# Kernel optimization log

Measured on AMD Instinct MI355X. Metric: run time of the kernel, lower is better.

## Reference

```python
import jax, jax.numpy as jnp
import numpy as np

B, H, L = 8, 256, 16384

def setup_inputs() -> dict:
    key = jax.random.key(0)
    k1, k2, k3 = jax.random.split(key, 3)
    u = jax.random.normal(k1, (B, H, L), dtype=jnp.float32)
    # SSM convolution kernel (H, L); small scale to keep tanh unsaturated
    k = jax.random.normal(k2, (H, L), dtype=jnp.float32) * 0.02
    # D feedthrough parameter (H, H); forward only uses its diagonal via einsum 'hh,bhl->bhl'
    D = jax.random.normal(k3, (H, H), dtype=jnp.float32)
    return {"u": u, "k": k, "D": D}

def reference(u, k, D):
    # circular FFT convolution: y = ifft(fft(u) * fft(k)).real
    u_s = jnp.fft.fft(u, axis=-1)          # (B,H,L) complex64
    k_s = jnp.fft.fft(k, axis=-1)          # (H,L)   complex64
    y = jnp.fft.ifft(u_s * k_s[None], axis=-1).real
    # D feedthrough: einsum 'hh,bhl->bhl' uses only diag(D)
    y = y + jnp.einsum('hh,bhl->bhl', D, u)
    return jnp.tanh(y)
```

## Files before the change

### kernel.cpp

```cpp
#include <hip/hip_runtime.h>
#include <math.h>

#define FFT_N 16384
#define NT 512
#define B_DIM 8
#define H_DIM 256

#define REGION 2048
#define RW (REGION + (REGION >> 5))
#define PAD(x) ((x) + ((x) >> 5))

#define WAVE_LDS_FENCE() do {                                   \
    __builtin_amdgcn_sched_barrier(0);                          \
    asm volatile("s_waitcnt lgkmcnt(0)" ::: "memory");          \
    __builtin_amdgcn_sched_barrier(0);                          \
} while (0)

__device__ __forceinline__ float2 cmul(float2 a, float2 b) {
    return make_float2(a.x * b.x - a.y * b.y, a.x * b.y + a.y * b.x);
}
__device__ __forceinline__ float2 cadd(float2 a, float2 b) { return make_float2(a.x + b.x, a.y + b.y); }
__device__ __forceinline__ float2 csub(float2 a, float2 b) { return make_float2(a.x - b.x, a.y - b.y); }
__device__ __forceinline__ float2 mulnegi(float2 z) { return make_float2(z.y, -z.x); }
__device__ __forceinline__ float2 mulposi(float2 z) { return make_float2(-z.y, z.x); }

__device__ __forceinline__ void bfly4(float2& a, float2& b, float2& c, float2& d,
                                      float2 w1, float2 w2, float2 w3) {
    float2 apc = cadd(a, c), amc = csub(a, c);
    float2 bpd = cadd(b, d), bmd = csub(b, d);
    float2 nib = mulnegi(bmd);
    a = cadd(apc, bpd);
    b = cmul(csub(apc, bpd), w2);
    c = cmul(cadd(amc, nib), w1);
    d = cmul(csub(amc, nib), w3);
}
__device__ __forceinline__ void bfly4_nw(float2& a, float2& b, float2& c, float2& d) {
    float2 apc = cadd(a, c), amc = csub(a, c);
    float2 bpd = cadd(b, d), bmd = csub(b, d);
    float2 nib = mulnegi(bmd);
    a = cadd(apc, bpd);
    b = csub(apc, bpd);
    c = cadd(amc, nib);
    d = csub(amc, nib);
}
__device__ __forceinline__ void ibfly4(float2& a, float2& b, float2& c, float2& d,
                                       float2 w1t, float2 w2t) {
    float2 w1 = make_float2(w1t.x, -w1t.y);
    float2 w2 = make_float2(w2t.x, -w2t.y);
    float2 bt = cmul(b, w2), dt = cmul(d, w2);
    float2 A = cadd(a, bt), Bb = csub(a, bt);
    float2 C = cadd(c, dt), Dd = csub(c, dt);
    float2 Cw = cmul(C, w1);
    float2 Dw = mulposi(cmul(Dd, w1));
    a = cadd(A, Cw);  c = csub(A, Cw);
    b = cadd(Bb, Dw); d = csub(Bb, Dw);
}
__device__ __forceinline__ void ibfly4_nw(float2& a, float2& b, float2& c, float2& d) {
    float2 A = cadd(a, b), Bb = csub(a, b);
    float2 C = cadd(c, d), Dd = csub(c, d);
    float2 Dw = mulposi(Dd);
    a = cadd(A, C);  c = csub(A, C);
    b = cadd(Bb, Dw); d = csub(Bb, Dw);
}

__device__ __forceinline__ void fwd_g01_half(float2 rh[16], const int t, const int par,
                                             const float2* __restrict__ tw) {
#pragma unroll
    for (int m0 = 0; m0 < 4; ++m0) {
        const int i = t + 512 * par + 1024 * m0;
        bfly4(rh[m0], rh[m0 + 4], rh[m0 + 8], rh[m0 + 12], tw[i], tw[2 * i], tw[3 * i]);
    }
    {
        const int ig = (t + 512 * par) * 4;
        const float2 w1 = tw[ig], w2 = tw[2 * ig], w3 = tw[3 * ig];
#pragma unroll
        for (int a = 0; a < 4; ++a)
            bfly4(rh[4 * a], rh[4 * a + 1], rh[4 * a + 2], rh[4 * a + 3], w1, w2, w3);
    }
}
__device__ __forceinline__ void inv_g01_half(float2 rh[16], const int t, const int par,
                                             const float2* __restrict__ tw) {
    {
        const int ig = (t + 512 * par) * 4;
        const float2 w1 = tw[ig], w2 = tw[2 * ig];
#pragma unroll
        for (int a = 0; a < 4; ++a)
            ibfly4(rh[4 * a], rh[4 * a + 1], rh[4 * a + 2], rh[4 * a + 3], w1, w2);
    }
#pragma unroll
    for (int m0 = 0; m0 < 4; ++m0) {
        const int i = t + 512 * par + 1024 * m0;
        ibfly4(rh[m0], rh[m0 + 4], rh[m0 + 8], rh[m0 + 12], tw[i], tw[2 * i]);
    }
}

__device__ __forceinline__ void fwd_mid_half(float2 rh[16], float* ldsx, float* ldsy,
                                             const int w, const int l, const int s,
                                             const float2* __restrict__ tw) {
#pragma unroll
    for (int jj = 0; jj < 16; ++jj) {
        const int a = w * RW + PAD(1024 * s + 64 * jj + l);
        rh[jj].x = ldsx[a]; rh[jj].y = ldsy[a];
    }
#pragma unroll
    for (int j0 = 0; j0 < 4; ++j0) {
        const int i1 = 1024 * j0 + 16 * l;
        bfly4(rh[j0], rh[j0 + 4], rh[j0 + 8], rh[j0 + 12], tw[i1], tw[2 * i1], tw[3 * i1]);
    }
    {
        const int i2 = 64 * l;
        const float2 w1 = tw[i2], w2 = tw[2 * i2], w3 = tw[3 * i2];
#pragma unroll
        for (int g = 0; g < 4; ++g)
            bfly4(rh[4 * g], rh[4 * g + 1], rh[4 * g + 2], rh[4 * g + 3], w1, w2, w3);
    }
#pragma unroll
    for (int jj = 0; jj < 16; ++jj) {
        const int a = w * RW + PAD(1024 * s + 64 * jj + l);
        ldsx[a] = rh[jj].x; ldsy[a] = rh[jj].y;
    }
    WAVE_LDS_FENCE();
    {
        const int lo = 64 * (l >> 2) + (l & 3);
#pragma unroll
        for (int jj = 0; jj < 16; ++jj) {
            const int a = w * RW + PAD(1024 * s + lo + 4 * jj);
            rh[jj].x = ldsx[a]; rh[jj].y = ldsy[a];
        }
    }
#pragma unroll
    for (int j0 = 0; j0 < 4; ++j0) {
        const int i3 = 1024 * j0 + 256 * (l & 3);
        bfly4(rh[j0], rh[j0 + 4], rh[j0 + 8], rh[j0 + 12], tw[i3], tw[2 * i3], tw[3 * i3]);
    }
    {
        const int i4 = 1024 * (l & 3);
        const float2 w1 = tw[i4], w2 = tw[2 * i4], w3 = tw[3 * i4];
#pragma unroll
        for (int g = 0; g < 4; ++g)
            bfly4(rh[4 * g], rh[4 * g + 1], rh[4 * g + 2], rh[4 * g + 3], w1, w2, w3);
    }
    {
        const int lo = 64 * (l >> 2) + (l & 3);
#pragma unroll
        for (int jj = 0; jj < 16; ++jj) {
            const int a = w * RW + PAD(1024 * s + lo + 4 * jj);
            ldsx[a] = rh[jj].x; ldsy[a] = rh[jj].y;
        }
    }
    WAVE_LDS_FENCE();
#pragma unroll
    for (int jj = 0; jj < 16; ++jj) {
        const int a = w * RW + PAD(1024 * s + 16 * l + jj);
        rh[jj].x = ldsx[a]; rh[jj].y = ldsy[a];
    }
#pragma unroll
    for (int g = 0; g < 4; ++g)
        bfly4_nw(rh[4 * g], rh[4 * g + 1], rh[4 * g + 2], rh[4 * g + 3]);
}

__device__ __forceinline__ void conv_mid_fused(float* ldsx, float* ldsy,
                                               const int t, const int w, const int l,
                                               const float4* __restrict__ kf4,
                                               const float invN,
                                               const float2* __restrict__ tw) {
    float2 r0[16], r1[16];
#pragma unroll
    for (int jj = 0; jj < 16; ++jj) {
        const int a0 = w * RW + PAD(64 * jj + l);
        const int a1 = w * RW + PAD(1024 + 64 * jj + l);
        r0[jj].x = ldsx[a0]; r0[jj].y = ldsy[a0];
        r1[jj].x = ldsx[a1]; r1[jj].y = ldsy[a1];
    }
#pragma unroll
    for (int j0 = 0; j0 < 4; ++j0) {
        const int i1 = 1024 * j0 + 16 * l;
        const float2 w1 = tw[i1], w2 = tw[2 * i1], w3 = tw[3 * i1];
        bfly4(r0[j0], r0[j0 + 4], r0[j0 + 8], r0[j0 + 12], w1, w2, w3);
        bfly4(r1[j0], r1[j0 + 4], r1[j0 + 8], r1[j0 + 12], w1, w2, w3);
    }
    {
        const int i2 = 64 * l;
        const float2 w1 = tw[i2], w2 = tw[2 * i2], w3 = tw[3 * i2];
#pragma unroll
        for (int g = 0; g < 4; ++g) {
            bfly4(r0[4 * g], r0[4 * g + 1], r0[4 * g + 2], r0[4 * g + 3], w1, w2, w3);
            bfly4(r1[4 * g], r1[4 * g + 1], r1[4 * g + 2], r1[4 * g + 3], w1, w2, w3);
        }
    }
#pragma unroll
    for (int jj = 0; jj < 16; ++jj) {
        const int a0 = w * RW + PAD(64 * jj + l);
        const int a1 = w * RW + PAD(1024 + 64 * jj + l);
        ldsx[a0] = r0[jj].x; ldsy[a0] = r0[jj].y;
        ldsx[a1] = r1[jj].x; ldsy[a1] = r1[jj].y;
    }
    WAVE_LDS_FENCE();
    {
        const int lo = 64 * (l >> 2) + (l & 3);
#pragma unroll
        for (int jj = 0; jj < 16; ++jj) {
            const int a0 = w * RW + PAD(lo + 4 * jj);
            const int a1 = w * RW + PAD(1024 + lo + 4 * jj);
            r0[jj].x = ldsx[a0]; r0[jj].y = ldsy[a0];
            r1[jj].x = ldsx[a1]; r1[jj].y = ldsy[a1];
        }
    }
#pragma unroll
    for (int j0 = 0; j0 < 4; ++j0) {
        const int i3 = 1024 * j0 + 256 * (l & 3);
        const float2 w1 = tw[i3], w2 = tw[2 * i3], w3 = tw[3 * i3];
        bfly4(r0[j0], r0[j0 + 4], r0[j0 + 8], r0[j0 + 12], w1, w2, w3);
        bfly4(r1[j0], r1[j0 + 4], r1[j0 + 8], r1[j0 + 12], w1, w2, w3);
    }
    {
        const int i4 = 1024 * (l & 3);
        const float2 w1 = tw[i4], w2 = tw[2 * i4], w3 = tw[3 * i4];
#pragma unroll
        for (int g = 0; g < 4; ++g) {
            bfly4(r0[4 * g], r0[4 * g + 1], r0[4 * g + 2], r0[4 * g + 3], w1, w2, w3);
            bfly4(r1[4 * g], r1[4 * g + 1], r1[4 * g + 2], r1[4 * g + 3], w1, w2, w3);
        }
    }
    {
        const int lo = 64 * (l >> 2) + (l & 3);
#pragma unroll
        for (int jj = 0; jj < 16; ++jj) {
            const int a0 = w * RW + PAD(lo + 4 * jj);
            const int a1 = w * RW + PAD(1024 + lo + 4 * jj);
            ldsx[a0] = r0[jj].x; ldsy[a0] = r0[jj].y;
            ldsx[a1] = r1[jj].x; ldsy[a1] = r1[jj].y;
        }
    }
    WAVE_LDS_FENCE();
#pragma unroll
    for (int jj = 0; jj < 16; ++jj) {
        const int a0 = w * RW + PAD(16 * l + jj);
        const int a1 = w * RW + PAD(1024 + 16 * l + jj);
        r0[jj].x = ldsx[a0]; r0[jj].y = ldsy[a0];
        r1[jj].x = ldsx[a1]; r1[jj].y = ldsy[a1];
    }
#pragma unroll
    for (int g = 0; g < 4; ++g) {
        bfly4_nw(r0[4 * g], r0[4 * g + 1], r0[4 * g + 2], r0[4 * g + 3]);
        bfly4_nw(r1[4 * g], r1[4 * g + 1], r1[4 * g + 2], r1[4 * g + 3]);
    }
#pragma unroll
    for (int q = 0; q < 8; ++q) {
        const float4 k0 = kf4[16 * t + q];
        const float4 k1 = kf4[16 * t + 8 + q];
        float2 z;
        z = r0[2 * q];
        r0[2 * q]     = make_float2((z.x * k0.x - z.y * k0.y) * invN, (z.x * k0.y + z.y * k0.x) * invN);
        z = r0[2 * q + 1];
        r0[2 * q + 1] = make_float2((z.x * k0.z - z.y * k0.w) * invN, (z.x * k0.w + z.y * k0.z) * invN);
        z = r1[2 * q];
        r1[2 * q]     = make_float2((z.x * k1.x - z.y * k1.y) * invN, (z.x * k1.y + z.y * k1.x) * invN);
        z = r1[2 * q + 1];
        r1[2 * q + 1] = make_float2((z.x * k1.z - z.y * k1.w) * invN, (z.x * k1.w + z.y * k1.z) * invN);
    }
#pragma unroll
    for (int g = 0; g < 4; ++g) {
        ibfly4_nw(r0[4 * g], r0[4 * g + 1], r0[4 * g + 2], r0[4 * g + 3]);
        ibfly4_nw(r1[4 * g], r1[4 * g + 1], r1[4 * g + 2], r1[4 * g + 3]);
    }
#pragma unroll
    for (int jj = 0; jj < 16; ++jj) {
        const int a0 = w * RW + PAD(16 * l + jj);
        const int a1 = w * RW + PAD(1024 + 16 * l + jj);
        ldsx[a0] = r0[jj].x; ldsy[a0] = r0[jj].y;
        ldsx[a1] = r1[jj].x; ldsy[a1] = r1[jj].y;
    }
    WAVE_LDS_FENCE();
    {
        const int lo = 64 * (l >> 2) + (l & 3);
#pragma unroll
        for (int jj = 0; jj < 16; ++jj) {
            const int a0 = w * RW + PAD(lo + 4 * jj);
            const int a1 = w * RW + PAD(1024 + lo + 4 * jj);
            r0[jj].x = ldsx[a0]; r0[jj].y = ldsy[a0];
            r1[jj].x = ldsx[a1]; r1[jj].y = ldsy[a1];
        }
    }
    {
        const int i4 = 1024 * (l & 3);
        const float2 w1 = tw[i4], w2 = tw[2 * i4];
#pragma unroll
        for (int g = 0; g < 4; ++g) {
            ibfly4(r0[4 * g], r0[4 * g + 1], r0[4 * g + 2], r0[4 * g + 3], w1, w2);
            ibfly4(r1[4 * g], r1[4 * g + 1], r1[4 * g + 2], r1[4 * g + 3], w1, w2);
        }
    }
#pragma unroll
    for (int j0 = 0; j0 < 4; ++j0) {
        const int i3 = 1024 * j0 + 256 * (l & 3);
        const float2 w1 = tw[i3], w2 = tw[2 * i3];
        ibfly4(r0[j0], r0[j0 + 4], r0[j0 + 8], r0[j0 + 12], w1, w2);
        ibfly4(r1[j0], r1[j0 + 4], r1[j0 + 8], r1[j0 + 12], w1, w2);
    }
    {
        const int lo = 64 * (l >> 2) + (l & 3);
#pragma unroll
        for (int jj = 0; jj < 16; ++jj) {
            const int a0 = w * RW + PAD(lo + 4 * jj);
            const int a1 = w * RW + PAD(1024 + lo + 4 * jj);
            ldsx[a0] = r0[jj].x; ldsy[a0] = r0[jj].y;
            ldsx[a1] = r1[jj].x; ldsy[a1] = r1[jj].y;
        }
    }
    WAVE_LDS_FENCE();
#pragma unroll
    for (int jj = 0; jj < 16; ++jj) {
        const int a0 = w * RW + PAD(64 * jj + l);
        const int a1 = w * RW + PAD(1024 + 64 * jj + l);
        r0[jj].x = ldsx[a0]; r0[jj].y = ldsy[a0];
        r1[jj].x = ldsx[a1]; r1[jj].y = ldsy[a1];
    }
    {
        const int i2 = 64 * l;
        const float2 w1 = tw[i2], w2 = tw[2 * i2];
#pragma unroll
        for (int g = 0; g < 4; ++g) {
            ibfly4(r0[4 * g], r0[4 * g + 1], r0[4 * g + 2], r0[4 * g + 3], w1, w2);
            ibfly4(r1[4 * g], r1[4 * g + 1], r1[4 * g + 2], r1[4 * g + 3], w1, w2);
        }
    }
#pragma unroll
    for (int j0 = 0; j0 < 4; ++j0) {
        const int i1 = 1024 * j0 + 16 * l;
        const float2 w1 = tw[i1], w2 = tw[2 * i1];
        ibfly4(r0[j0], r0[j0 + 4], r0[j0 + 8], r0[j0 + 12], w1, w2);
        ibfly4(r1[j0], r1[j0 + 4], r1[j0 + 8], r1[j0 + 12], w1, w2);
    }
#pragma unroll
    for (int jj = 0; jj < 16; ++jj) {
        const int a0 = w * RW + PAD(64 * jj + l);
        const int a1 = w * RW + PAD(1024 + 64 * jj + l);
        ldsx[a0] = r0[jj].x; ldsy[a0] = r0[jj].y;
        ldsx[a1] = r1[jj].x; ldsy[a1] = r1[jj].y;
    }
}

__device__ __forceinline__ float ftanh(float x) {
    float e = __expf(2.0f * x);
    return 1.0f - 2.0f * __builtin_amdgcn_rcpf(e + 1.0f);
}

__global__ void twiddle_init(float2* __restrict__ tw) {
    int t = blockIdx.x * blockDim.x + threadIdx.x;
    if (t < FFT_N) {
        float ang = -2.0f * 3.14159265358979323846f * (float)t / (float)FFT_N;
        float sv, cv;
        sincosf(ang, &sv, &cv);
        tw[t] = make_float2(cv, sv);
    }
}

__global__ __launch_bounds__(NT) void kfft_kernel(const float* __restrict__ k,
                                                  const float* __restrict__ D,
                                                  const float2* __restrict__ tw,
                                                  float2* __restrict__ Kf) {
    __shared__ float ldsx[8 * RW];
    __shared__ float ldsy[8 * RW];
    const int h = blockIdx.x;
    const int t = threadIdx.x;
    const int w = t >> 6, l = t & 63;
    const float* krow = k + (size_t)h * FFT_N;
    const float dh = D[h * (H_DIM + 1)];
#pragma unroll
    for (int par = 0; par < 2; ++par) {
        float2 rh[16];
#pragma unroll
        for (int m = 0; m < 16; ++m)
            rh[m] = make_float2(krow[t + 512 * par + 1024 * m], 0.f);
        if (par == 0 && t == 0) rh[0].x += dh;
        fwd_g01_half(rh, t, par, tw);
#pragma unroll
        for (int m = 0; m < 16; ++m) {
            const int e = t + 512 * par + 1024 * m;
            const int a = (e >> 11) * RW + PAD(e & 2047);
            ldsx[a] = rh[m].x; ldsy[a] = rh[m].y;
        }
    }
    __syncthreads();
    float4* out4 = (float4*)(Kf + (size_t)h * FFT_N);
#pragma unroll
    for (int s = 0; s < 2; ++s) {
        float2 rh[16];
        fwd_mid_half(rh, ldsx, ldsy, w, l, s, tw);
#pragma unroll
        for (int q = 0; q < 8; ++q)
            out4[16 * t + 8 * s + q] =
                make_float4(rh[2 * q].x, rh[2 * q].y, rh[2 * q + 1].x, rh[2 * q + 1].y);
    }
}

__global__ __launch_bounds__(NT) void conv_kernel(const float* __restrict__ u,
                                                  const float2* __restrict__ tw,
                                                  const float2* __restrict__ Kf,
                                                  float* __restrict__ out) {
    __shared__ float ldsx[8 * RW];
    __shared__ float ldsy[8 * RW];
    const int raw = blockIdx.x;
    const int vb = ((raw & 7) << 7) + (raw >> 3);
    const int h = vb >> 2;
    const int p = vb & 3;
    const int t = threadIdx.x;
    const int w = t >> 6, l = t & 63;
    const size_t row0 = ((size_t)(2 * p) * H_DIM + h) * FFT_N;
    const size_t row1 = row0 + (size_t)H_DIM * FFT_N;
    const float* u0 = u + row0;
    const float* u1 = u + row1;

#pragma unroll
    for (int par = 0; par < 2; ++par) {
        float2 rh[16];
#pragma unroll
        for (int m = 0; m < 16; ++m) {
            const int n = t + 512 * par + 1024 * m;
            rh[m] = make_float2(u0[n], u1[n]);
        }
        fwd_g01_half(rh, t, par, tw);
#pragma unroll
        for (int m = 0; m < 16; ++m) {
            const int e = t + 512 * par + 1024 * m;
            const int a = (e >> 11) * RW + PAD(e & 2047);
            ldsx[a] = rh[m].x; ldsy[a] = rh[m].y;
        }
    }
    __syncthreads();

    conv_mid_fused(ldsx, ldsy, t, w, l,
                   (const float4*)(Kf + (size_t)h * FFT_N), 1.0f / (float)FFT_N, tw);
    __syncthreads();

    float* o0 = out + row0;
    float* o1 = out + row1;
#pragma unroll
    for (int par = 0; par < 2; ++par) {
        float2 rh[16];
#pragma unroll
        for (int m = 0; m < 16; ++m) {
            const int e = t + 512 * par + 1024 * m;
            const int a = (e >> 11) * RW + PAD(e & 2047);
            rh[m].x = ldsx[a]; rh[m].y = ldsy[a];
        }
        inv_g01_half(rh, t, par, tw);
#pragma unroll
        for (int m = 0; m < 16; ++m) {
            const int n = t + 512 * par + 1024 * m;
            o0[n] = ftanh(rh[m].x);
            o1[n] = ftanh(rh[m].y);
        }
    }
}

extern "C" void kernel_launch(void* const* d_in, const int* in_sizes, int n_in,
                              void* d_out, int out_size, void* d_ws, size_t ws_size,
                              hipStream_t stream) {
    const float* u = (const float*)d_in[0];
    const float* k = (const float*)d_in[1];
    const float* D = (const float*)d_in[2];
    float* out = (float*)d_out;

    float2* tw = (float2*)d_ws;
    float2* Kf = tw + FFT_N;

    twiddle_init<<<FFT_N / 256, 256, 0, stream>>>(tw);
    kfft_kernel<<<H_DIM, NT, 0, stream>>>(k, D, tw, Kf);
    conv_kernel<<<(B_DIM / 2) * H_DIM, NT, 0, stream>>>(u, tw, Kf, out);
}
```

Baseline: 200.4 us.

## Drop wave LDS fences, fold 1/N into kernel spectrum, prefetch Kf early

Removes the explicit per-wave s_waitcnt/sched_barrier fences between LDS write and read phases and leaves ordering to the compiler's own waitcnt insertion. Moves the 1/N scaling into the precomputed kernel spectrum so the pointwise multiply in the conv kernel does fewer multiplies. Issues early touch loads of the Kf row at kernel start, kept alive with an empty asm, so the spectrum is pulled into cache while the forward FFT runs. Removing the fences relies on the compiler to keep correct LDS ordering within a wave, and the prefetch adds a few registers.

After: 209.8 us. +4.7%, slower.

```diff
diff --git a/kernel.cpp b/kernel.cpp
--- a/kernel.cpp
+++ b/kernel.cpp
@@ -10,11 +10,6 @@
 #define RW (REGION + (REGION >> 5))
 #define PAD(x) ((x) + ((x) >> 5))
 
-#define WAVE_LDS_FENCE() do {                                   \
-    __builtin_amdgcn_sched_barrier(0);                          \
-    asm volatile("s_waitcnt lgkmcnt(0)" ::: "memory");          \
-    __builtin_amdgcn_sched_barrier(0);                          \
-} while (0)
 
 __device__ __forceinline__ float2 cmul(float2 a, float2 b) {
     return make_float2(a.x * b.x - a.y * b.y, a.x * b.y + a.y * b.x);
@@ -119,7 +114,6 @@
         const int a = w * RW + PAD(1024 * s + 64 * jj + l);
         ldsx[a] = rh[jj].x; ldsy[a] = rh[jj].y;
     }
-    WAVE_LDS_FENCE();
     {
         const int lo = 64 * (l >> 2) + (l & 3);
 #pragma unroll
@@ -148,7 +142,6 @@
             ldsx[a] = rh[jj].x; ldsy[a] = rh[jj].y;
         }
     }
-    WAVE_LDS_FENCE();
 #pragma unroll
     for (int jj = 0; jj < 16; ++jj) {
         const int a = w * RW + PAD(1024 * s + 16 * l + jj);
@@ -162,7 +155,7 @@
 __device__ __forceinline__ void conv_mid_fused(float* ldsx, float* ldsy,
                                                const int t, const int w, const int l,
                                                const float4* __restrict__ kf4,
-                                               const float invN,
+                                               float tch0, float tch1, float tch2, float tch3,
                                                const float2* __restrict__ tw) {
     float2 r0[16], r1[16];
 #pragma unroll
@@ -195,7 +188,6 @@
         ldsx[a0] = r0[jj].x; ldsy[a0] = r0[jj].y;
         ldsx[a1] = r1[jj].x; ldsy[a1] = r1[jj].y;
     }
-    WAVE_LDS_FENCE();
     {
         const int lo = 64 * (l >> 2) + (l & 3);
 #pragma unroll
@@ -232,7 +224,6 @@
             ldsx[a1] = r1[jj].x; ldsy[a1] = r1[jj].y;
         }
     }
-    WAVE_LDS_FENCE();
 #pragma unroll
     for (int jj = 0; jj < 16; ++jj) {
         const int a0 = w * RW + PAD(16 * l + jj);
@@ -245,19 +236,20 @@
         bfly4_nw(r0[4 * g], r0[4 * g + 1], r0[4 * g + 2], r0[4 * g + 3]);
         bfly4_nw(r1[4 * g], r1[4 * g + 1], r1[4 * g + 2], r1[4 * g + 3]);
     }
+    asm volatile("" :: "v"(tch0), "v"(tch1), "v"(tch2), "v"(tch3));
 #pragma unroll
     for (int q = 0; q < 8; ++q) {
         const float4 k0 = kf4[16 * t + q];
         const float4 k1 = kf4[16 * t + 8 + q];
         float2 z;
         z = r0[2 * q];
-        r0[2 * q]     = make_float2((z.x * k0.x - z.y * k0.y) * invN, (z.x * k0.y + z.y * k0.x) * invN);
+        r0[2 * q]     = make_float2(z.x * k0.x - z.y * k0.y, z.x * k0.y + z.y * k0.x);
         z = r0[2 * q + 1];
-        r0[2 * q + 1] = make_float2((z.x * k0.z - z.y * k0.w) * invN, (z.x * k0.w + z.y * k0.z) * invN);
+        r0[2 * q + 1] = make_float2(z.x * k0.z - z.y * k0.w, z.x * k0.w + z.y * k0.z);
         z = r1[2 * q];
-        r1[2 * q]     = make_float2((z.x * k1.x - z.y * k1.y) * invN, (z.x * k1.y + z.y * k1.x) * invN);
+        r1[2 * q]     = make_float2(z.x * k1.x - z.y * k1.y, z.x * k1.y + z.y * k1.x);
         z = r1[2 * q + 1];
-        r1[2 * q + 1] = make_float2((z.x * k1.z - z.y * k1.w) * invN, (z.x * k1.w + z.y * k1.z) * invN);
+        r1[2 * q + 1] = make_float2(z.x * k1.z - z.y * k1.w, z.x * k1.w + z.y * k1.z);
     }
 #pragma unroll
     for (int g = 0; g < 4; ++g) {
@@ -271,7 +263,6 @@
         ldsx[a0] = r0[jj].x; ldsy[a0] = r0[jj].y;
         ldsx[a1] = r1[jj].x; ldsy[a1] = r1[jj].y;
     }
-    WAVE_LDS_FENCE();
     {
         const int lo = 64 * (l >> 2) + (l & 3);
 #pragma unroll
@@ -308,7 +299,6 @@
             ldsx[a1] = r1[jj].x; ldsy[a1] = r1[jj].y;
         }
     }
-    WAVE_LDS_FENCE();
 #pragma unroll
     for (int jj = 0; jj < 16; ++jj) {
         const int a0 = w * RW + PAD(64 * jj + l);
@@ -383,6 +373,7 @@
         }
     }
     __syncthreads();
+    const float invN = 1.0f / (float)FFT_N;
     float4* out4 = (float4*)(Kf + (size_t)h * FFT_N);
 #pragma unroll
     for (int s = 0; s < 2; ++s) {
@@ -391,7 +382,8 @@
 #pragma unroll
         for (int q = 0; q < 8; ++q)
             out4[16 * t + 8 * s + q] =
-                make_float4(rh[2 * q].x, rh[2 * q].y, rh[2 * q + 1].x, rh[2 * q + 1].y);
+                make_float4(rh[2 * q].x * invN, rh[2 * q].y * invN,
+                            rh[2 * q + 1].x * invN, rh[2 * q + 1].y * invN);
     }
 }
 
@@ -412,6 +404,12 @@
     const float* u0 = u + row0;
     const float* u1 = u + row1;
 
+    const float* kfw = (const float*)(Kf + (size_t)h * FFT_N);
+    const float tch0 = kfw[16 * t];
+    const float tch1 = kfw[16 * (t + 512)];
+    const float tch2 = kfw[16 * (t + 1024)];
+    const float tch3 = kfw[16 * (t + 1536)];
+
 #pragma unroll
     for (int par = 0; par < 2; ++par) {
         float2 rh[16];
@@ -431,7 +429,8 @@
     __syncthreads();
 
     conv_mid_fused(ldsx, ldsy, t, w, l,
-                   (const float4*)(Kf + (size_t)h * FFT_N), 1.0f / (float)FFT_N, tw);
+                   (const float4*)(Kf + (size_t)h * FFT_N),
+                   tch0, tch1, tch2, tch3, tw);
     __syncthreads();
 
     float* o0 = out + row0;
```
